# Optimization experiments

Hardware: AMD Instinct MI355X
Metric: run time of the kernel (lower is better)

## Reference

```python
import jax, jax.numpy as jnp
import numpy as np

BN_EPS = 1e-5


def setup_inputs() -> dict:
    key = jax.random.key(0)
    k1, k2, k3 = jax.random.split(key, 3)
    B, T, I, H = 64, 2048, 128, 128
    x = jax.random.normal(k1, (B, T, I), dtype=jnp.float32)
    W = jax.random.normal(k2, (H, I), dtype=jnp.float32) * (1.0 / np.sqrt(I))
    # orthogonal recurrent matrix, as in nn.init.orthogonal_
    V = jnp.linalg.qr(jax.random.normal(k3, (H, H), dtype=jnp.float32))[0]
    gamma = jnp.ones((H,), dtype=jnp.float32)
    beta = jnp.zeros((H,), dtype=jnp.float32)
    return {"x": x, "W": W, "V": V, "gamma": gamma, "beta": beta}


def reference(x, W, V, gamma, beta):
    B, T, H = x.shape[0], x.shape[1], W.shape[0]
    # feedforward projection: [B,T,I] @ [H,I]^T -> [B,T,H]
    Wx = jnp.einsum('bti,hi->bth', x, W)
    # batchnorm (training mode) over flattened (B*T, H)
    flat = Wx.reshape(B * T, H)
    mean = jnp.mean(flat, axis=0)
    var = jnp.var(flat, axis=0)
    Wx = ((flat - mean) * jax.lax.rsqrt(var + BN_EPS) * gamma + beta).reshape(B, T, H)
    # sequential recurrence: yt = sigmoid(Wx_t + yt @ V^T)
    Vt = V.T

    def step(yt, wx_t):
        yt = jax.nn.sigmoid(wx_t + yt @ Vt)
        return yt, yt

    y0 = jnp.zeros((B, H), dtype=Wx.dtype)
    _, ys = jax.lax.scan(step, y0, jnp.swapaxes(Wx, 0, 1))  # ys: [T,B,H]
    return jnp.swapaxes(ys, 0, 1)  # [B,T,H]
```

## Files before the change

kernel.cpp:

```cpp
#include <hip/hip_runtime.h>
#include <cstdint>
#include <cstddef>

#define N_ROWS 131072
#define T_LEN 2048
#define B_BATCH 64
#define H_DIM 128
#define GEMM_GRID 1024
#define GEMM_ROWS 128
#define WND 8
#define LOG2E 1.4426950408889634f

#define VEC_SWZ 160

typedef _Float16 half2_t __attribute__((ext_vector_type(2)));

__device__ __forceinline__ float dpp_xor1(float x) {
  int i = __float_as_int(x);
  return __int_as_float(__builtin_amdgcn_update_dpp(i, i, 0xB1, 0xF, 0xF, true));
}
__device__ __forceinline__ float dpp_xor2(float x) {
  int i = __float_as_int(x);
  return __int_as_float(__builtin_amdgcn_update_dpp(i, i, 0x4E, 0xF, 0xF, true));
}
__device__ __forceinline__ float dpp_mirror8(float x) {
  int i = __float_as_int(x);
  return __int_as_float(__builtin_amdgcn_update_dpp(i, i, 0x141, 0xF, 0xF, true));
}

__device__ __forceinline__ float dot4(float4 a, float4 b, float acc) {
  return fmaf(a.w, b.w, fmaf(a.z, b.z, fmaf(a.y, b.y, fmaf(a.x, b.x, acc))));
}

#define DOT32(P, VR)                                                          \
  {                                                                           \
    float c0 = dot4(a4, VR[4], dot4(a0, VR[0], 0.f));                         \
    float c1 = dot4(a5, VR[5], dot4(a1, VR[1], 0.f));                         \
    float c2 = dot4(a6, VR[6], dot4(a2, VR[2], 0.f));                         \
    float c3 = dot4(a7, VR[7], dot4(a3, VR[3], 0.f));                         \
    P = (c0 + c1) + (c2 + c3);                                                \
  }
#define REDUCE2(S, p0, p1)                                                    \
  float S;                                                                    \
  {                                                                           \
    float q = p0 + dpp_xor1(p1);                                              \
    S = q + dpp_xor2(q);                                                      \
  }

__global__ __launch_bounds__(256) void gemm_bn_kernel(
    const float* __restrict__ x, const float* __restrict__ W,
    float* __restrict__ Wx, float* __restrict__ stats)
{
  const int tid = threadIdx.x;
  const int hq = tid >> 2;
  const int ks = tid & 3;
  const int k0 = ks << 5;
  const int h_own = hq + ((ks & 1) << 6);
  const int h_alt = hq + (((ks & 1) ^ 1) << 6);

  float4 Wr[2][8];
  {
    const float4* w0 = reinterpret_cast<const float4*>(W + (size_t)h_own * H_DIM + k0);
    const float4* w1 = reinterpret_cast<const float4*>(W + (size_t)h_alt * H_DIM + k0);
#pragma unroll
    for (int j = 0; j < 8; ++j) { Wr[0][j] = w0[j]; Wr[1][j] = w1[j]; }
  }

  __shared__ __align__(16) float xs[2][WND * VEC_SWZ];

  const int r0 = blockIdx.x * GEMM_ROWS;
  const int sr = tid >> 5;
  const int c4 = tid & 31;
  const int sdst = sr * VEC_SWZ + (c4 >> 2) * 20 + (c4 & 3) * 4;

  *reinterpret_cast<float4*>(&xs[0][sdst]) =
      *reinterpret_cast<const float4*>(&x[(size_t)(r0 + sr) * H_DIM + (c4 << 2)]);
  __syncthreads();

  float sum = 0.f, sq = 0.f;

  for (int wnd = 0; wnd < GEMM_ROWS; wnd += WND) {
    const int bw = (wnd >> 3) & 1;
    const bool more = (wnd + WND < GEMM_ROWS);
    float4 sv;
    if (more)
      sv = *reinterpret_cast<const float4*>(
          &x[(size_t)(r0 + wnd + WND + sr) * H_DIM + (c4 << 2)]);

#pragma unroll
    for (int r = 0; r < WND; ++r) {
      const float* xp = &xs[bw][r * VEC_SWZ + ks * 40];
      const float4* xa = reinterpret_cast<const float4*>(xp);
      const float4* xb = reinterpret_cast<const float4*>(xp + 20);
      float4 a0 = xa[0], a1 = xa[1], a2 = xa[2], a3 = xa[3];
      float4 a4 = xb[0], a5 = xb[1], a6 = xb[2], a7 = xb[3];
      float p0, p1;
      DOT32(p0, Wr[0]); DOT32(p1, Wr[1]);
      REDUCE2(s, p0, p1);
      if (ks < 2) {
        Wx[(size_t)(r0 + wnd + r) * H_DIM + h_own] = s;
        sum += s;
        sq = fmaf(s, s, sq);
      }
    }
    if (more) *reinterpret_cast<float4*>(&xs[bw ^ 1][sdst]) = sv;
    __syncthreads();
  }
  if (ks < 2) {
    atomicAdd(&stats[h_own], sum);
    atomicAdd(&stats[H_DIM + h_own], sq);
  }
}

__global__ void bn_finalize_kernel(float* ws, const float* __restrict__ gamma,
                                   const float* __restrict__ beta)
{
  const int h = threadIdx.x;
  const float invN = 1.0f / (float)N_ROWS;
  float mean = ws[h] * invN;
  float e2   = ws[H_DIM + h] * invN;
  float var  = e2 - mean * mean;
  float scl  = gamma[h] * rsqrtf(var + 1e-5f);
  ws[2 * H_DIM + h] = scl;
  ws[3 * H_DIM + h] = beta[h] - mean * scl;
}

__global__ __launch_bounds__(256) void rnn_kernel(
    const float* __restrict__ V, float* __restrict__ out,
    const float* __restrict__ ws)
{
  const int tid = threadIdx.x;
  const int hq = tid >> 3;
  const int l7 = tid & 7;
  const int g  = (l7 & 3) ^ (3 * ((l7 >> 2) & 1));
  const int h_own = hq + (g << 5);
  const bool wr = (tid & 4) == 0;

  half2_t Vh[4][8];
#pragma unroll
  for (int j = 0; j < 4; ++j) {
    const int hrow = hq + (((unsigned)(j ^ g)) << 5);
    const float* vp = V + (size_t)hrow * H_DIM + (l7 << 4);
#pragma unroll
    for (int i = 0; i < 8; ++i) {
      half2_t h;
      h.x = (_Float16)(-LOG2E * vp[2 * i]);
      h.y = (_Float16)(-LOG2E * vp[2 * i + 1]);
      Vh[j][i] = h;
    }
  }
  const float scl2 = ws[2 * H_DIM + h_own] * (-LOG2E);
  const float shf2 = ws[3 * H_DIM + h_own] * (-LOG2E);

  __shared__ __align__(16) _Float16 ylds[2][H_DIM];

  float* outb = out + (size_t)blockIdx.x * T_LEN * H_DIM;

  if (tid < H_DIM) { ylds[0][tid] = (_Float16)0.f; ylds[1][tid] = (_Float16)0.f; }

  float wxp[WND];
  if (wr) {
#pragma unroll
    for (int u = 0; u < WND; ++u)
      wxp[u] = fmaf(outb[(size_t)u * H_DIM + h_own], scl2, shf2);
  } else {
#pragma unroll
    for (int u = 0; u < WND; ++u) wxp[u] = 0.f;
  }
  __syncthreads();

  float yreg[WND];

  for (int w = 0; w < T_LEN; w += WND) {
    const bool more = (w + WND < T_LEN);
    float wxn[WND];
    if (more && wr) {
#pragma unroll
      for (int u = 0; u < WND; ++u)
        wxn[u] = outb[(size_t)(w + WND + u) * H_DIM + h_own];
    } else {
#pragma unroll
      for (int u = 0; u < WND; ++u) wxn[u] = 0.f;
    }

#pragma unroll
    for (int u = 0; u < WND; ++u) {
      const int t = w + u;
      const uint4* yv = reinterpret_cast<const uint4*>(&ylds[t & 1][l7 << 4]);
      uint4 w0 = yv[0], w1 = yv[1];
      half2_t y2[8];
      y2[0] = __builtin_bit_cast(half2_t, w0.x);
      y2[1] = __builtin_bit_cast(half2_t, w0.y);
      y2[2] = __builtin_bit_cast(half2_t, w0.z);
      y2[3] = __builtin_bit_cast(half2_t, w0.w);
      y2[4] = __builtin_bit_cast(half2_t, w1.x);
      y2[5] = __builtin_bit_cast(half2_t, w1.y);
      y2[6] = __builtin_bit_cast(half2_t, w1.z);
      y2[7] = __builtin_bit_cast(half2_t, w1.w);

      float a0 = 0.f, a1 = 0.f, a2 = 0.f, a3 = 0.f;
#pragma unroll
      for (int i = 0; i < 8; ++i) {
        a0 = __builtin_amdgcn_fdot2(y2[i], Vh[0][i], a0, false);
        a1 = __builtin_amdgcn_fdot2(y2[i], Vh[1][i], a1, false);
        a2 = __builtin_amdgcn_fdot2(y2[i], Vh[2][i], a2, false);
        a3 = __builtin_amdgcn_fdot2(y2[i], Vh[3][i], a3, false);
      }
      float b0 = a0 + dpp_xor1(a1);
      float b1 = a2 + dpp_xor1(a3);
      float c  = b0 + dpp_xor2(b1);
      float red = c + dpp_mirror8(c);
      const float spp = red + wxp[u];
      const float y = __builtin_amdgcn_rcpf(1.0f + __builtin_amdgcn_exp2f(spp));
      if (wr) ylds[(t & 1) ^ 1][h_own] = (_Float16)y;
      yreg[u] = y;
      asm volatile("s_waitcnt lgkmcnt(0)\n\ts_barrier" ::: "memory");
    }

    if (wr) {
#pragma unroll
      for (int u = 0; u < WND; ++u)
        outb[(size_t)(w + u) * H_DIM + h_own] = yreg[u];
    }
#pragma unroll
    for (int u = 0; u < WND; ++u) wxp[u] = fmaf(wxn[u], scl2, shf2);
  }
}

extern "C" void kernel_launch(void* const* d_in, const int* in_sizes, int n_in,
                              void* d_out, int out_size, void* d_ws, size_t ws_size,
                              hipStream_t stream)
{
  (void)in_sizes; (void)n_in; (void)out_size; (void)ws_size;
  const float* x     = (const float*)d_in[0];
  const float* W     = (const float*)d_in[1];
  const float* V     = (const float*)d_in[2];
  const float* gamma = (const float*)d_in[3];
  const float* beta  = (const float*)d_in[4];
  float* out = (float*)d_out;
  float* ws  = (float*)d_ws;

  hipMemsetAsync(ws, 0, 2 * H_DIM * sizeof(float), stream);
  gemm_bn_kernel<<<GEMM_GRID, 256, 0, stream>>>(x, W, out, ws);
  bn_finalize_kernel<<<1, H_DIM, 0, stream>>>(ws, gamma, beta);
  rnn_kernel<<<B_BATCH, 256, 0, stream>>>(V, out, ws);
}
```

Baseline: 539.5 us.

## Rewrite feedforward GEMM with fp16 MFMA and swizzled LDS tile

The projection GEMM now converts each 128-row x tile to fp16 in a swizzled shared-memory buffer and holds W fragments in fp16 registers. It computes the tile with 16x16x32 MFMA instructions instead of scalar fp32 FMAs. BatchNorm partial sums are reduced across lanes with permlane swaps before the atomics. This targets the compute cost of the GEMM stage, at the price of fp16 rounding of x and W, which shifts the BN statistics slightly; the recurrence kernel is only tidied.

```diff
diff --git a/kernel.cpp b/kernel.cpp
--- a/kernel.cpp
+++ b/kernel.cpp
@@ -7,13 +7,13 @@
 #define B_BATCH 64
 #define H_DIM 128
 #define GEMM_GRID 1024
-#define GEMM_ROWS 128
 #define WND 8
 #define LOG2E 1.4426950408889634f
 
-#define VEC_SWZ 160
-
 typedef _Float16 half2_t __attribute__((ext_vector_type(2)));
+typedef _Float16 half8_t __attribute__((ext_vector_type(8)));
+typedef float f32x4_t __attribute__((ext_vector_type(4)));
+typedef int int2_t __attribute__((ext_vector_type(2)));
 
 __device__ __forceinline__ float dpp_xor1(float x) {
   int i = __float_as_int(x);
@@ -28,87 +28,113 @@
   return __int_as_float(__builtin_amdgcn_update_dpp(i, i, 0x141, 0xF, 0xF, true));
 }
 
-__device__ __forceinline__ float dot4(float4 a, float4 b, float acc) {
-  return fmaf(a.w, b.w, fmaf(a.z, b.z, fmaf(a.y, b.y, fmaf(a.x, b.x, acc))));
-}
-
-#define DOT32(P, VR)                                                          \
-  {                                                                           \
-    float c0 = dot4(a4, VR[4], dot4(a0, VR[0], 0.f));                         \
-    float c1 = dot4(a5, VR[5], dot4(a1, VR[1], 0.f));                         \
-    float c2 = dot4(a6, VR[6], dot4(a2, VR[2], 0.f));                         \
-    float c3 = dot4(a7, VR[7], dot4(a3, VR[3], 0.f));                         \
-    P = (c0 + c1) + (c2 + c3);                                                \
-  }
-#define REDUCE2(S, p0, p1)                                                    \
-  float S;                                                                    \
-  {                                                                           \
-    float q = p0 + dpp_xor1(p1);                                              \
-    S = q + dpp_xor2(q);                                                      \
-  }
+__device__ __forceinline__ float permlane16_sum(float x) {
+  int i = __float_as_int(x);
+  int2_t r = __builtin_amdgcn_permlane16_swap(i, i, false, false);
+  return __int_as_float(r.x) + __int_as_float(r.y);
+}
+__device__ __forceinline__ float permlane32_sum(float x) {
+  int i = __float_as_int(x);
+  int2_t r = __builtin_amdgcn_permlane32_swap(i, i, false, false);
+  return __int_as_float(r.x) + __int_as_float(r.y);
+}
+
+__device__ __forceinline__ float sigmoid2_fast(float spp) {
+  return __builtin_amdgcn_rcpf(1.0f + __builtin_amdgcn_exp2f(spp));
+}
 
 __global__ __launch_bounds__(256) void gemm_bn_kernel(
     const float* __restrict__ x, const float* __restrict__ W,
     float* __restrict__ Wx, float* __restrict__ stats)
 {
-  const int tid = threadIdx.x;
-  const int hq = tid >> 2;
-  const int ks = tid & 3;
-  const int k0 = ks << 5;
-  const int h_own = hq + ((ks & 1) << 6);
-  const int h_alt = hq + (((ks & 1) ^ 1) << 6);
-
-  float4 Wr[2][8];
+  const int tid  = threadIdx.x;
+  const int lane = tid & 63;
+  const int wv   = tid >> 6;
+  const int l15  = lane & 15;
+  const int kg   = lane >> 4;
+  const int r0   = blockIdx.x * 128;
+
+  half8_t Bf[2][4];
+#pragma unroll
+  for (int n = 0; n < 2; ++n) {
+    const int col = wv * 32 + n * 16 + l15;
+    const float* wp = W + (size_t)col * H_DIM;
+#pragma unroll
+    for (int k = 0; k < 4; ++k) {
+      const float* w8 = wp + k * 32 + kg * 8;
+      half8_t b;
+#pragma unroll
+      for (int i = 0; i < 8; ++i) b[i] = (_Float16)w8[i];
+      Bf[n][k] = b;
+    }
+  }
+
+  __shared__ __align__(16) _Float16 xs[128 * 128];
   {
-    const float4* w0 = reinterpret_cast<const float4*>(W + (size_t)h_own * H_DIM + k0);
-    const float4* w1 = reinterpret_cast<const float4*>(W + (size_t)h_alt * H_DIM + k0);
-#pragma unroll
-    for (int j = 0; j < 8; ++j) { Wr[0][j] = w0[j]; Wr[1][j] = w1[j]; }
-  }
-
-  __shared__ __align__(16) float xs[2][WND * VEC_SWZ];
-
-  const int r0 = blockIdx.x * GEMM_ROWS;
-  const int sr = tid >> 5;
-  const int c4 = tid & 31;
-  const int sdst = sr * VEC_SWZ + (c4 >> 2) * 20 + (c4 & 3) * 4;
-
-  *reinterpret_cast<float4*>(&xs[0][sdst]) =
-      *reinterpret_cast<const float4*>(&x[(size_t)(r0 + sr) * H_DIM + (c4 << 2)]);
+    const int row = tid >> 1;
+    const int hf  = tid & 1;
+    const float* xp = x + (size_t)(r0 + row) * H_DIM + hf * 64;
+    const int swz = (row & 7) << 4;
+    char* base = reinterpret_cast<char*>(xs) + row * 256;
+#pragma unroll
+    for (int c = 0; c < 8; ++c) {
+      float4 v0 = *reinterpret_cast<const float4*>(xp + c * 8);
+      float4 v1 = *reinterpret_cast<const float4*>(xp + c * 8 + 4);
+      half8_t h;
+      h[0] = (_Float16)v0.x; h[1] = (_Float16)v0.y;
+      h[2] = (_Float16)v0.z; h[3] = (_Float16)v0.w;
+      h[4] = (_Float16)v1.x; h[5] = (_Float16)v1.y;
+      h[6] = (_Float16)v1.z; h[7] = (_Float16)v1.w;
+      const int X = hf * 128 + c * 16;
+      *reinterpret_cast<half8_t*>(base + (X ^ swz)) = h;
+    }
+  }
   __syncthreads();
 
-  float sum = 0.f, sq = 0.f;
-
-  for (int wnd = 0; wnd < GEMM_ROWS; wnd += WND) {
-    const int bw = (wnd >> 3) & 1;
-    const bool more = (wnd + WND < GEMM_ROWS);
-    float4 sv;
-    if (more)
-      sv = *reinterpret_cast<const float4*>(
-          &x[(size_t)(r0 + wnd + WND + sr) * H_DIM + (c4 << 2)]);
-
-#pragma unroll
-    for (int r = 0; r < WND; ++r) {
-      const float* xp = &xs[bw][r * VEC_SWZ + ks * 40];
-      const float4* xa = reinterpret_cast<const float4*>(xp);
-      const float4* xb = reinterpret_cast<const float4*>(xp + 20);
-      float4 a0 = xa[0], a1 = xa[1], a2 = xa[2], a3 = xa[3];
-      float4 a4 = xb[0], a5 = xb[1], a6 = xb[2], a7 = xb[3];
-      float p0, p1;
-      DOT32(p0, Wr[0]); DOT32(p1, Wr[1]);
-      REDUCE2(s, p0, p1);
-      if (ks < 2) {
-        Wx[(size_t)(r0 + wnd + r) * H_DIM + h_own] = s;
-        sum += s;
-        sq = fmaf(s, s, sq);
-      }
-    }
-    if (more) *reinterpret_cast<float4*>(&xs[bw ^ 1][sdst]) = sv;
-    __syncthreads();
-  }
-  if (ks < 2) {
-    atomicAdd(&stats[h_own], sum);
-    atomicAdd(&stats[H_DIM + h_own], sq);
+  f32x4_t C[8][2];
+#pragma unroll
+  for (int m = 0; m < 8; ++m)
+#pragma unroll
+    for (int n = 0; n < 2; ++n)
+      C[m][n] = (f32x4_t){0.f, 0.f, 0.f, 0.f};
+
+#pragma unroll
+  for (int m = 0; m < 8; ++m) {
+    const int row = m * 16 + l15;
+    const char* rbase = reinterpret_cast<const char*>(xs) + row * 256;
+    const int swz = (row & 7) << 4;
+#pragma unroll
+    for (int k = 0; k < 4; ++k) {
+      const int X = k * 64 + kg * 16;
+      half8_t a = *reinterpret_cast<const half8_t*>(rbase + (X ^ swz));
+      C[m][0] = __builtin_amdgcn_mfma_f32_16x16x32_f16(a, Bf[0][k], C[m][0], 0, 0, 0);
+      C[m][1] = __builtin_amdgcn_mfma_f32_16x16x32_f16(a, Bf[1][k], C[m][1], 0, 0, 0);
+    }
+  }
+
+  float sum0 = 0.f, sq0 = 0.f, sum1 = 0.f, sq1 = 0.f;
+#pragma unroll
+  for (int m = 0; m < 8; ++m) {
+#pragma unroll
+    for (int j = 0; j < 4; ++j) {
+      const int row = r0 + m * 16 + kg * 4 + j;
+      const float v0 = C[m][0][j];
+      const float v1 = C[m][1][j];
+      Wx[(size_t)row * H_DIM + wv * 32 + l15]      = v0;
+      Wx[(size_t)row * H_DIM + wv * 32 + 16 + l15] = v1;
+      sum0 += v0; sq0 = fmaf(v0, v0, sq0);
+      sum1 += v1; sq1 = fmaf(v1, v1, sq1);
+    }
+  }
+  float s0 = permlane32_sum(permlane16_sum(sum0));
+  float q0 = permlane32_sum(permlane16_sum(sq0));
+  float s1 = permlane32_sum(permlane16_sum(sum1));
+  float q1 = permlane32_sum(permlane16_sum(sq1));
+  if (lane < 16) {
+    atomicAdd(&stats[wv * 32 + lane],              s0);
+    atomicAdd(&stats[H_DIM + wv * 32 + lane],      q0);
+    atomicAdd(&stats[wv * 32 + 16 + lane],         s1);
+    atomicAdd(&stats[H_DIM + wv * 32 + 16 + lane], q1);
   }
 }
 
@@ -211,7 +237,7 @@
       float c  = b0 + dpp_xor2(b1);
       float red = c + dpp_mirror8(c);
       const float spp = red + wxp[u];
-      const float y = __builtin_amdgcn_rcpf(1.0f + __builtin_amdgcn_exp2f(spp));
+      const float y = sigmoid2_fast(spp);
       if (wr) ylds[(t & 1) ^ 1][h_own] = (_Float16)y;
       yreg[u] = y;
       asm volatile("s_waitcnt lgkmcnt(0)\n\ts_barrier" ::: "memory");
```

Result: faster. 519.2 us (-3.8%).
